# Optimization experiments

Hardware: AMD Instinct MI355X
Metric: run time of the kernel (lower is better)

The kernel has to match this reference:

```python
import jax, jax.numpy as jnp
import numpy as np

EMBED = 1024
HEADS = 16
HEAD_DIM = EMBED // HEADS


def setup_inputs() -> dict:
    key = jax.random.key(0)
    ks = jax.random.split(key, 8)
    N, S, E = 4, 2048, EMBED
    inp = {
        "queries": jax.random.normal(ks[0], (N, S, E), dtype=jnp.float32),
        "keys": jax.random.normal(ks[1], (N, S, E), dtype=jnp.float32),
        "values": jax.random.normal(ks[2], (N, S, E), dtype=jnp.float32),
        # projection weights, stored as (in, out) so y = x @ W
        "Wq": jax.random.normal(ks[3], (E, E), dtype=jnp.float32) / np.sqrt(E),
        "Wk": jax.random.normal(ks[4], (E, E), dtype=jnp.float32) / np.sqrt(E),
        "Wv": jax.random.normal(ks[5], (E, E), dtype=jnp.float32) / np.sqrt(E),
        "Wo": jax.random.normal(ks[6], (E, E), dtype=jnp.float32) / np.sqrt(E),
        "bo": jax.random.normal(ks[7], (E,), dtype=jnp.float32) * 0.01,
    }
    return inp


def reference(queries, keys, values, Wq, Wk, Wv, Wo, bo):
    N, Sq, E = queries.shape
    Sk = keys.shape[1]
    H, D = HEADS, HEAD_DIM
    # linear projections (no bias)
    q = (queries @ Wq).reshape(N, Sq, H, D)
    k = (keys @ Wk).reshape(N, Sk, H, D)
    v = (values @ Wv).reshape(N, Sk, H, D)
    # energy: [N, H, Sq, Sk]
    energy = jnp.einsum("nqhd,nkhd->nhqk", q, k)
    attn = jax.nn.softmax(energy / np.sqrt(D).astype(np.float32), axis=3)
    # out: [N, Sq, H, D] -> [N, Sq, E]
    out = jnp.einsum("nhqk,nkhd->nqhd", attn, v).reshape(N, Sq, E)
    return out @ Wo + bo
```

## Files before the change

kernel.cpp:

```cpp
#include <hip/hip_runtime.h>
#include <hip/hip_bf16.h>

typedef __bf16 bf16;
typedef bf16 bf16x4v __attribute__((ext_vector_type(4)));
typedef bf16 bf16x8 __attribute__((ext_vector_type(8)));
typedef float f32x4 __attribute__((ext_vector_type(4)));
typedef float f32x16 __attribute__((ext_vector_type(16)));
typedef unsigned int uint;
typedef unsigned short ushort;

static constexpr int E   = 1024;
static constexpr int SEQ = 2048;
static constexpr int NB  = 4;
static constexpr int M   = NB * SEQ;

__device__ __forceinline__ void async16(const void* g, void* l) {
  __builtin_amdgcn_global_load_lds(
      (const __attribute__((address_space(1))) void*)g,
      (__attribute__((address_space(3))) void*)l, 16, 0, 0);
}

__device__ __forceinline__ uint pack2(float a, float b) {
  bf16 x = (bf16)a, y = (bf16)b;
  return (uint)__builtin_bit_cast(ushort, x) |
         ((uint)__builtin_bit_cast(ushort, y) << 16);
}

__global__ __launch_bounds__(256) void k_prep(const float* q_in, const float* k_in,
                                              const float* v_in,
                                              bf16* qc, bf16* kc, bf16* vc,
                                              const float* W0, const float* W1,
                                              const float* W2, const float* W3,
                                              bf16* T0, bf16* T1, bf16* T2, bf16* T3) {
  __shared__ float tile[64][65];
  const int bid = blockIdx.x, t = threadIdx.x;
  if (bid < 12288) {
    const int z = bid >> 12, x = bid & 4095;
    const float* src = z == 0 ? q_in : z == 1 ? k_in : v_in;
    bf16* dst        = z == 0 ? qc   : z == 1 ? kc   : vc;
    size_t i = (size_t)x * 256 + t;
    const float4* s = reinterpret_cast<const float4*>(src) + i * 2;
    float4 a = s[0], b = s[1];
    bf16x8 o;
    o[0] = (bf16)a.x; o[1] = (bf16)a.y; o[2] = (bf16)a.z; o[3] = (bf16)a.w;
    o[4] = (bf16)b.x; o[5] = (bf16)b.y; o[6] = (bf16)b.z; o[7] = (bf16)b.w;
    *reinterpret_cast<bf16x8*>(dst + i * 8) = o;
  } else {
    const int wid = bid - 12288;
    const int wz = wid >> 8, rem = wid & 255;
    const int bx = rem & 15, by = rem >> 4;
    const float* W = wz == 0 ? W0 : wz == 1 ? W1 : wz == 2 ? W2 : W3;
    bf16* WT       = wz == 0 ? T0 : wz == 1 ? T1 : wz == 2 ? T2 : T3;
    const int tx = t & 63, ty = t >> 6;
    const int nb = bx * 64, kb = by * 64;
#pragma unroll
    for (int r = 0; r < 16; ++r)
      tile[ty + r * 4][tx] = W[(size_t)(kb + ty + r * 4) * E + nb + tx];
    __syncthreads();
#pragma unroll
    for (int r = 0; r < 16; ++r)
      WT[(size_t)(nb + ty + r * 4) * E + kb + tx] = (bf16)tile[tx][ty + r * 4];
  }
}

__global__ __launch_bounds__(256) void k_gemmP(const bf16* A0, const bf16* A1,
                                               const bf16* A2,
                                               const bf16* B0, const bf16* B1,
                                               const bf16* B2,
                                               bf16* O0, bf16* O1, bf16* O2) {
  __shared__ __align__(16) bf16 As[2][128 * 32];
  __shared__ __align__(16) bf16 Bs[2][128 * 32];
  const int z = blockIdx.z;
  const bf16* A  = z == 0 ? A0 : z == 1 ? A1 : A2;
  const bf16* BT = z == 0 ? B0 : z == 1 ? B1 : B2;
  const int t = threadIdx.x;
  const int l = t & 63, w = t >> 6;
  const int lo = l & 15, hi = l >> 4;
  const int wm = w >> 1, wn = w & 1;
  const int m0 = blockIdx.x * 128, n0 = blockIdx.y * 128;
  f32x4 acc[4][4] = {};

  const int r0 = t >> 2, s0 = t & 3;
  const bf16* ga0 = A + (size_t)(m0 + r0) * E + s0 * 8;
  const bf16* ga1 = ga0 + (size_t)64 * E;
  const bf16* gb0 = BT + (size_t)(n0 + r0) * E + s0 * 8;
  const bf16* gb1 = gb0 + (size_t)64 * E;

  auto stage = [&](int buf, int kk) {
    char* la = (char*)As[buf] + t * 16;
    char* lb = (char*)Bs[buf] + t * 16;
    async16(ga0 + kk, la);
    async16(ga1 + kk, la + 4096);
    async16(gb0 + kk, lb);
    async16(gb1 + kk, lb + 4096);
  };

  stage(0, 0);
  __syncthreads();
  int cur = 0;
  for (int kk = 0; kk < E; kk += 32) {
    if (kk + 32 < E) stage(cur ^ 1, kk + 32);
    const bf16* AsC = As[cur];
    const bf16* BsC = Bs[cur];
    bf16x8 af[4], bfr[4];
#pragma unroll
    for (int mi = 0; mi < 4; ++mi)
      af[mi] = *(const bf16x8*)&AsC[(wm * 64 + mi * 16 + lo) * 32 + hi * 8];
#pragma unroll
    for (int ni = 0; ni < 4; ++ni)
      bfr[ni] = *(const bf16x8*)&BsC[(wn * 64 + ni * 16 + lo) * 32 + hi * 8];
    __builtin_amdgcn_s_setprio(1);
#pragma unroll
    for (int mi = 0; mi < 4; ++mi)
#pragma unroll
      for (int ni = 0; ni < 4; ++ni)
        acc[mi][ni] = __builtin_amdgcn_mfma_f32_16x16x32_bf16(af[mi], bfr[ni],
                                                              acc[mi][ni], 0, 0, 0);
    __builtin_amdgcn_s_setprio(0);
    __syncthreads();
    cur ^= 1;
  }

  const int mrow = m0 + wm * 64, ncol = n0 + wn * 64;
  if (z == 2) {
#pragma unroll
    for (int mi = 0; mi < 4; ++mi) {
      int mrow_ = mrow + mi * 16 + hi * 4;
      int nb_ = mrow_ >> 11, sidx = mrow_ & 2047;
#pragma unroll
      for (int ni = 0; ni < 4; ++ni) {
        int col = ncol + ni * 16 + lo;
        bf16x4v v4;
#pragma unroll
        for (int j = 0; j < 4; ++j) v4[j] = (bf16)acc[mi][ni][j];
        *(bf16x4v*)(O2 + ((size_t)(nb_ * 16 + (col >> 6)) * 64 + (col & 63)) * SEQ + sidx) = v4;
      }
    }
  } else {
    const float sc = (z == 0) ? 0.18033688011112042f : 1.0f;
    bf16* C = z == 0 ? O0 : O1;
#pragma unroll
    for (int mi = 0; mi < 4; ++mi)
#pragma unroll
      for (int ni = 0; ni < 4; ++ni)
#pragma unroll
        for (int i = 0; i < 4; ++i)
          C[(size_t)(mrow + mi * 16 + hi * 4 + i) * E + ncol + ni * 16 + lo] =
              (bf16)(acc[mi][ni][i] * sc);
  }
}

__global__ __launch_bounds__(256) void k_gemmO(const bf16* __restrict__ A,
                                               const bf16* __restrict__ BT,
                                               float* __restrict__ C,
                                               const float* __restrict__ bias) {
  __shared__ __align__(16) bf16 As[2][128 * 32];
  __shared__ __align__(16) bf16 Bs[2][128 * 32];
  const int t = threadIdx.x;
  const int l = t & 63, w = t >> 6;
  const int lo = l & 15, hi = l >> 4;
  const int wm = w >> 1, wn = w & 1;
  const int m0 = blockIdx.x * 128, n0 = blockIdx.y * 128;
  f32x4 acc[4][4] = {};

  const int r0 = t >> 2, s0 = t & 3;
  const bf16* ga0 = A + (size_t)(m0 + r0) * E + s0 * 8;
  const bf16* ga1 = ga0 + (size_t)64 * E;
  const bf16* gb0 = BT + (size_t)(n0 + r0) * E + s0 * 8;
  const bf16* gb1 = gb0 + (size_t)64 * E;

  auto stage = [&](int buf, int kk) {
    char* la = (char*)As[buf] + t * 16;
    char* lb = (char*)Bs[buf] + t * 16;
    async16(ga0 + kk, la);
    async16(ga1 + kk, la + 4096);
    async16(gb0 + kk, lb);
    async16(gb1 + kk, lb + 4096);
  };

  stage(0, 0);
  __syncthreads();
  int cur = 0;
  for (int kk = 0; kk < E; kk += 32) {
    if (kk + 32 < E) stage(cur ^ 1, kk + 32);
    const bf16* AsC = As[cur];
    const bf16* BsC = Bs[cur];
    bf16x8 af[4], bfr[4];
#pragma unroll
    for (int mi = 0; mi < 4; ++mi)
      af[mi] = *(const bf16x8*)&AsC[(wm * 64 + mi * 16 + lo) * 32 + hi * 8];
#pragma unroll
    for (int ni = 0; ni < 4; ++ni)
      bfr[ni] = *(const bf16x8*)&BsC[(wn * 64 + ni * 16 + lo) * 32 + hi * 8];
    __builtin_amdgcn_s_setprio(1);
#pragma unroll
    for (int mi = 0; mi < 4; ++mi)
#pragma unroll
      for (int ni = 0; ni < 4; ++ni)
        acc[mi][ni] = __builtin_amdgcn_mfma_f32_16x16x32_bf16(af[mi], bfr[ni],
                                                              acc[mi][ni], 0, 0, 0);
    __builtin_amdgcn_s_setprio(0);
    __syncthreads();
    cur ^= 1;
  }

  const int mrow = m0 + wm * 64, ncol = n0 + wn * 64;
  float bv[4];
#pragma unroll
  for (int ni = 0; ni < 4; ++ni) bv[ni] = bias[ncol + ni * 16 + lo];
#pragma unroll
  for (int mi = 0; mi < 4; ++mi)
#pragma unroll
    for (int ni = 0; ni < 4; ++ni)
#pragma unroll
      for (int i = 0; i < 4; ++i)
        C[(size_t)(mrow + mi * 16 + hi * 4 + i) * E + ncol + ni * 16 + lo] =
            acc[mi][ni][i] + bv[ni];
}

__global__ __launch_bounds__(256, 2) void k_attn(const bf16* __restrict__ Qp,
                                                 const bf16* __restrict__ Kp,
                                                 const bf16* __restrict__ Vt,
                                                 bf16* __restrict__ Z) {
  __shared__ __align__(16) bf16 KV[2][2][64 * 64];
  const int t = threadIdx.x, l = t & 63, w = t >> 6;
  const int qq = l & 31, hi = l >> 5, l7 = l & 7;
  const int p = blockIdx.x;
  const int lswz = (p & 7) * 64 + (p >> 3);
  const int qb = lswz & 7, nh = lswz >> 3;
  const int n = nh >> 4, h = nh & 15;
  const int q0w = qb * 256 + w * 64;
  const int krow = (qq & 0x13) | ((qq & 4) << 1) | ((qq & 8) >> 1);

  bf16x8 qf[2][4];
#pragma unroll
  for (int j = 0; j < 2; ++j) {
    const bf16* qrow = Qp + (size_t)(n * SEQ + q0w + j * 32 + qq) * E + h * 64;
#pragma unroll
    for (int ks = 0; ks < 4; ++ks) qf[j][ks] = *(const bf16x8*)(qrow + ks * 16 + hi * 8);
  }

  const bf16* kbase = Kp + (size_t)n * SEQ * E + h * 64;
  const bf16* vbase = Vt + (size_t)nh * 64 * SEQ;
  const int r_st = t >> 3, s_st = t & 7;
  const int gs = (s_st ^ (r_st & 7)) * 8;

  auto stage = [&](int buf, int kt) {
    char* lk = (char*)KV[buf][0] + t * 16;
    char* lv = (char*)KV[buf][1] + t * 16;
    async16(kbase + (size_t)(kt + r_st) * E + gs, lk);
    async16(kbase + (size_t)(kt + r_st + 32) * E + gs, lk + 4096);
    async16(vbase + (size_t)r_st * SEQ + kt + gs, lv);
    async16(vbase + (size_t)(r_st + 32) * SEQ + kt + gs, lv + 4096);
  };

  f32x16 oacc[2][2] = {};
  float l_r[2] = {0.f, 0.f};

  stage(0, 0);
  __syncthreads();
  int cur = 0;
  for (int kt = 0; kt < SEQ; kt += 64) {
    if (kt + 64 < SEQ) stage(cur ^ 1, kt + 64);
    const bf16* KsC = KV[cur][0];
    const bf16* VsC = KV[cur][1];

    f32x16 sacc[2][2];
    __builtin_amdgcn_s_setprio(1);
#pragma unroll
    for (int kb = 0; kb < 2; ++kb) {
      bf16x8 kfr[4];
#pragma unroll
      for (int ks = 0; ks < 4; ++ks)
        kfr[ks] = *(const bf16x8*)(KsC + (kb * 32 + krow) * 64 + (((ks * 2 + hi) ^ (krow & 7)) * 8));
#pragma unroll
      for (int j = 0; j < 2; ++j) {
        f32x16 a = {};
#pragma unroll
        for (int ks = 0; ks < 4; ++ks)
          a = __builtin_amdgcn_mfma_f32_32x32x16_bf16(kfr[ks], qf[j][ks], a, 0, 0, 0);
        sacc[j][kb] = a;
      }
    }
    __builtin_amdgcn_s_setprio(0);

    uint wv[2][2][8];
#pragma unroll
    for (int j = 0; j < 2; ++j) {
      float rs = 0.f;
#pragma unroll
      for (int kb = 0; kb < 2; ++kb) {
        float pv[16];
#pragma unroll
        for (int r = 0; r < 16; ++r) {
          float e = __builtin_amdgcn_exp2f(sacc[j][kb][r]);
          pv[r] = e;
          rs += e;
        }
#pragma unroll
        for (int i = 0; i < 8; ++i) wv[j][kb][i] = pack2(pv[2 * i], pv[2 * i + 1]);
      }
      l_r[j] += rs;
    }

    __builtin_amdgcn_s_setprio(1);
#pragma unroll
    for (int d = 0; d < 2; ++d)
#pragma unroll
      for (int kb = 0; kb < 2; ++kb)
#pragma unroll
        for (int ks2 = 0; ks2 < 2; ++ks2) {
          const int ks = kb * 2 + ks2;
          bf16x8 vf = *(const bf16x8*)(VsC + (d * 32 + qq) * 64 + (((ks * 2 + hi) ^ l7) * 8));
#pragma unroll
          for (int j = 0; j < 2; ++j) {
            bf16x8 pf;
            uint* pp = (uint*)&pf;
            pp[0] = wv[j][kb][ks2 * 4 + 0];
            pp[1] = wv[j][kb][ks2 * 4 + 1];
            pp[2] = wv[j][kb][ks2 * 4 + 2];
            pp[3] = wv[j][kb][ks2 * 4 + 3];
            oacc[j][d] = __builtin_amdgcn_mfma_f32_32x32x16_bf16(vf, pf, oacc[j][d], 0, 0, 0);
          }
        }
    __builtin_amdgcn_s_setprio(0);
    __syncthreads();
    cur ^= 1;
  }

#pragma unroll
  for (int j = 0; j < 2; ++j) {
    const float lt = l_r[j] + __shfl_xor(l_r[j], 32);
    const float inv = 1.f / lt;
    bf16* zrow = Z + (size_t)(n * SEQ + q0w + j * 32 + qq) * E + h * 64;
#pragma unroll
    for (int d = 0; d < 2; ++d)
#pragma unroll
      for (int g = 0; g < 4; ++g) {
        bf16x4v v4;
#pragma unroll
        for (int jj = 0; jj < 4; ++jj) v4[jj] = (bf16)(oacc[j][d][g * 4 + jj] * inv);
        *(bf16x4v*)(zrow + d * 32 + g * 8 + hi * 4) = v4;
      }
  }
}

extern "C" void kernel_launch(void* const* d_in, const int* in_sizes, int n_in,
                              void* d_out, int out_size, void* d_ws, size_t ws_size,
                              hipStream_t stream) {
  const float* q_in = (const float*)d_in[0];
  const float* k_in = (const float*)d_in[1];
  const float* v_in = (const float*)d_in[2];
  const float* Wq   = (const float*)d_in[3];
  const float* Wk   = (const float*)d_in[4];
  const float* Wv   = (const float*)d_in[5];
  const float* Wo   = (const float*)d_in[6];
  const float* bo   = (const float*)d_in[7];

  char* ws = (char*)d_ws;
  const size_t SZ = (size_t)M * E * 2;
  bf16* qc   = (bf16*)(ws);
  bf16* kc   = (bf16*)(ws + SZ);
  bf16* vc   = (bf16*)(ws + 2 * SZ);
  bf16* qp   = (bf16*)(ws + 3 * SZ);
  bf16* kp   = (bf16*)(ws + 4 * SZ);
  bf16* vt   = (bf16*)(ws + 5 * SZ);
  bf16* zz   = (bf16*)(ws + 6 * SZ);
  bf16* wT   = (bf16*)(ws + 7 * SZ);
  bf16* wqT = wT;
  bf16* wkT = wT + (size_t)E * E;
  bf16* wvT = wT + 2 * (size_t)E * E;
  bf16* woT = wT + 3 * (size_t)E * E;

  dim3 b256(256);
  k_prep<<<dim3(13312), b256, 0, stream>>>(q_in, k_in, v_in, qc, kc, vc,
                                           Wq, Wk, Wv, Wo, wqT, wkT, wvT, woT);
  k_gemmP<<<dim3(64, 8, 3), b256, 0, stream>>>(qc, kc, vc, wqT, wkT, wvT,
                                               qp, kp, vt);
  k_attn<<<dim3(512), b256, 0, stream>>>(qp, kp, vt, zz);
  k_gemmO<<<dim3(64, 8), b256, 0, stream>>>(zz, woT, (float*)d_out, bo);
}
```

Measured before the change: 201.3 us.

## Split attention key sequence across two wave groups per block and merge via LDS

Doubles the attention block to 512 threads. Each group of four waves handles half of the key/value sequence with its own double-buffered LDS staging. At the end, the second half writes its partial outputs and row sums to LDS, and the first half adds them, normalizes and stores. This doubles the waves available per CU to hide latency on a grid that only fills two blocks per CU. The cost is more LDS per block, an extra merge step, and a tighter register budget from __launch_bounds__(512,4), which could cause spills.

Result: slower. 600.5 us (+198.4%).

```diff
diff --git a/kernel.cpp b/kernel.cpp
--- a/kernel.cpp
+++ b/kernel.cpp
@@ -218,18 +218,21 @@
             acc[mi][ni][i] + bv[ni];
 }
 
-__global__ __launch_bounds__(256, 2) void k_attn(const bf16* __restrict__ Qp,
+__global__ __launch_bounds__(512, 4) void k_attn(const bf16* __restrict__ Qp,
                                                  const bf16* __restrict__ Kp,
                                                  const bf16* __restrict__ Vt,
                                                  bf16* __restrict__ Z) {
-  __shared__ __align__(16) bf16 KV[2][2][64 * 64];
+  __shared__ __align__(16) char smem[65536];
   const int t = threadIdx.x, l = t & 63, w = t >> 6;
+  const int half = w >> 2, w4 = w & 3;
+  const int th = t & 255;
   const int qq = l & 31, hi = l >> 5, l7 = l & 7;
   const int p = blockIdx.x;
   const int lswz = (p & 7) * 64 + (p >> 3);
   const int qb = lswz & 7, nh = lswz >> 3;
   const int n = nh >> 4, h = nh & 15;
-  const int q0w = qb * 256 + w * 64;
+  const int q0w = qb * 256 + w4 * 64;
+  const int ktbase = half * (SEQ / 2);
   const int krow = (qq & 0x13) | ((qq & 4) << 1) | ((qq & 8) >> 1);
 
   bf16x8 qf[2][4];
@@ -242,16 +245,17 @@
 
   const bf16* kbase = Kp + (size_t)n * SEQ * E + h * 64;
   const bf16* vbase = Vt + (size_t)nh * 64 * SEQ;
-  const int r_st = t >> 3, s_st = t & 7;
+  const int r_st = th >> 3, s_st = th & 7;
   const int gs = (s_st ^ (r_st & 7)) * 8;
 
-  auto stage = [&](int buf, int kt) {
-    char* lk = (char*)KV[buf][0] + t * 16;
-    char* lv = (char*)KV[buf][1] + t * 16;
-    async16(kbase + (size_t)(kt + r_st) * E + gs, lk);
-    async16(kbase + (size_t)(kt + r_st + 32) * E + gs, lk + 4096);
-    async16(vbase + (size_t)r_st * SEQ + kt + gs, lv);
-    async16(vbase + (size_t)(r_st + 32) * SEQ + kt + gs, lv + 4096);
+  auto stage = [&](int buf, int ktl) {
+    char* lk = smem + half * 32768 + buf * 16384 + th * 16;
+    char* lv = lk + 8192;
+    const int ktg = ktbase + ktl;
+    async16(kbase + (size_t)(ktg + r_st) * E + gs, lk);
+    async16(kbase + (size_t)(ktg + r_st + 32) * E + gs, lk + 4096);
+    async16(vbase + (size_t)r_st * SEQ + ktg + gs, lv);
+    async16(vbase + (size_t)(r_st + 32) * SEQ + ktg + gs, lv + 4096);
   };
 
   f32x16 oacc[2][2] = {};
@@ -260,10 +264,10 @@
   stage(0, 0);
   __syncthreads();
   int cur = 0;
-  for (int kt = 0; kt < SEQ; kt += 64) {
-    if (kt + 64 < SEQ) stage(cur ^ 1, kt + 64);
-    const bf16* KsC = KV[cur][0];
-    const bf16* VsC = KV[cur][1];
+  for (int ktl = 0; ktl < SEQ / 2; ktl += 64) {
+    if (ktl + 64 < SEQ / 2) stage(cur ^ 1, ktl + 64);
+    const bf16* KsC = (const bf16*)(smem + half * 32768 + cur * 16384);
+    const bf16* VsC = (const bf16*)(smem + half * 32768 + cur * 16384 + 8192);
 
     f32x16 sacc[2][2];
     __builtin_amdgcn_s_setprio(1);
@@ -328,20 +332,39 @@
     cur ^= 1;
   }
 
+  float lt[2];
+#pragma unroll
+  for (int j = 0; j < 2; ++j) lt[j] = l_r[j] + __shfl_xor(l_r[j], 32);
+
+  float* Obuf = (float*)smem;
 #pragma unroll
   for (int j = 0; j < 2; ++j) {
-    const float lt = l_r[j] + __shfl_xor(l_r[j], 32);
-    const float inv = 1.f / lt;
-    bf16* zrow = Z + (size_t)(n * SEQ + q0w + j * 32 + qq) * E + h * 64;
-#pragma unroll
-    for (int d = 0; d < 2; ++d)
-#pragma unroll
-      for (int g = 0; g < 4; ++g) {
-        bf16x4v v4;
-#pragma unroll
-        for (int jj = 0; jj < 4; ++jj) v4[jj] = (bf16)(oacc[j][d][g * 4 + jj] * inv);
-        *(bf16x4v*)(zrow + d * 32 + g * 8 + hi * 4) = v4;
-      }
+    float* row = Obuf + (w4 * 64 + l) * 36;
+    if (half == 1) {
+      *(f32x16*)(row) = oacc[j][0];
+      *(f32x16*)(row + 16) = oacc[j][1];
+      row[32] = lt[j];
+    }
+    __syncthreads();
+    if (half == 0) {
+      f32x16 o1a = *(const f32x16*)(row);
+      f32x16 o1b = *(const f32x16*)(row + 16);
+      const float inv = 1.f / (lt[j] + row[32]);
+      f32x16 fo[2];
+      fo[0] = (oacc[j][0] + o1a) * inv;
+      fo[1] = (oacc[j][1] + o1b) * inv;
+      bf16* zrow = Z + (size_t)(n * SEQ + q0w + j * 32 + qq) * E + h * 64;
+#pragma unroll
+      for (int d = 0; d < 2; ++d)
+#pragma unroll
+        for (int g = 0; g < 4; ++g) {
+          bf16x4v v4;
+#pragma unroll
+          for (int jj = 0; jj < 4; ++jj) v4[jj] = (bf16)fo[d][g * 4 + jj];
+          *(bf16x4v*)(zrow + d * 32 + g * 8 + hi * 4) = v4;
+        }
+    }
+    if (j == 0) __syncthreads();
   }
 }
 
@@ -377,6 +400,6 @@
                                            Wq, Wk, Wv, Wo, wqT, wkT, wvT, woT);
   k_gemmP<<<dim3(64, 8, 3), b256, 0, stream>>>(qc, kc, vc, wqT, wkT, wvT,
                                                qp, kp, vt);
-  k_attn<<<dim3(512), b256, 0, stream>>>(qp, kp, vt, zz);
+  k_attn<<<dim3(512), dim3(512), 0, stream>>>(qp, kp, vt, zz);
   k_gemmO<<<dim3(64, 8), b256, 0, stream>>>(zz, woT, (float*)d_out, bo);
 }
```

## Fuse fp32-to-bf16 input conversion into projection GEMM A-operand loads

Applied to the files above, without the earlier changes.

Removes the separate pass that converts the fp32 query/key/value inputs to bf16. The projection GEMM now reads fp32 activations straight from global memory into registers and packs them to bf16 for the MFMA A operand, dropping A from shared memory. This saves a full write and re-read of three 8M-element bf16 buffers. In exchange, each block's A reads are uncached, per-wave fp32 register loads that are not shared through LDS, and these loads are not prefetched ahead of the compute.

After: 305.3 us. +51.7%, slower.

```diff
diff --git a/kernel.cpp b/kernel.cpp
--- a/kernel.cpp
+++ b/kernel.cpp
@@ -26,52 +26,34 @@
          ((uint)__builtin_bit_cast(ushort, y) << 16);
 }
 
-__global__ __launch_bounds__(256) void k_prep(const float* q_in, const float* k_in,
-                                              const float* v_in,
-                                              bf16* qc, bf16* kc, bf16* vc,
-                                              const float* W0, const float* W1,
+__global__ __launch_bounds__(256) void k_prep(const float* W0, const float* W1,
                                               const float* W2, const float* W3,
                                               bf16* T0, bf16* T1, bf16* T2, bf16* T3) {
   __shared__ float tile[64][65];
   const int bid = blockIdx.x, t = threadIdx.x;
-  if (bid < 12288) {
-    const int z = bid >> 12, x = bid & 4095;
-    const float* src = z == 0 ? q_in : z == 1 ? k_in : v_in;
-    bf16* dst        = z == 0 ? qc   : z == 1 ? kc   : vc;
-    size_t i = (size_t)x * 256 + t;
-    const float4* s = reinterpret_cast<const float4*>(src) + i * 2;
-    float4 a = s[0], b = s[1];
-    bf16x8 o;
-    o[0] = (bf16)a.x; o[1] = (bf16)a.y; o[2] = (bf16)a.z; o[3] = (bf16)a.w;
-    o[4] = (bf16)b.x; o[5] = (bf16)b.y; o[6] = (bf16)b.z; o[7] = (bf16)b.w;
-    *reinterpret_cast<bf16x8*>(dst + i * 8) = o;
-  } else {
-    const int wid = bid - 12288;
-    const int wz = wid >> 8, rem = wid & 255;
-    const int bx = rem & 15, by = rem >> 4;
-    const float* W = wz == 0 ? W0 : wz == 1 ? W1 : wz == 2 ? W2 : W3;
-    bf16* WT       = wz == 0 ? T0 : wz == 1 ? T1 : wz == 2 ? T2 : T3;
-    const int tx = t & 63, ty = t >> 6;
-    const int nb = bx * 64, kb = by * 64;
-#pragma unroll
-    for (int r = 0; r < 16; ++r)
-      tile[ty + r * 4][tx] = W[(size_t)(kb + ty + r * 4) * E + nb + tx];
-    __syncthreads();
-#pragma unroll
-    for (int r = 0; r < 16; ++r)
-      WT[(size_t)(nb + ty + r * 4) * E + kb + tx] = (bf16)tile[tx][ty + r * 4];
-  }
-}
-
-__global__ __launch_bounds__(256) void k_gemmP(const bf16* A0, const bf16* A1,
-                                               const bf16* A2,
+  const int wz = bid >> 8, rem = bid & 255;
+  const int bx = rem & 15, by = rem >> 4;
+  const float* W = wz == 0 ? W0 : wz == 1 ? W1 : wz == 2 ? W2 : W3;
+  bf16* WT       = wz == 0 ? T0 : wz == 1 ? T1 : wz == 2 ? T2 : T3;
+  const int tx = t & 63, ty = t >> 6;
+  const int nb = bx * 64, kb = by * 64;
+#pragma unroll
+  for (int r = 0; r < 16; ++r)
+    tile[ty + r * 4][tx] = W[(size_t)(kb + ty + r * 4) * E + nb + tx];
+  __syncthreads();
+#pragma unroll
+  for (int r = 0; r < 16; ++r)
+    WT[(size_t)(nb + ty + r * 4) * E + kb + tx] = (bf16)tile[tx][ty + r * 4];
+}
+
+__global__ __launch_bounds__(256) void k_gemmP(const float* A0, const float* A1,
+                                               const float* A2,
                                                const bf16* B0, const bf16* B1,
                                                const bf16* B2,
                                                bf16* O0, bf16* O1, bf16* O2) {
-  __shared__ __align__(16) bf16 As[2][128 * 32];
   __shared__ __align__(16) bf16 Bs[2][128 * 32];
   const int z = blockIdx.z;
-  const bf16* A  = z == 0 ? A0 : z == 1 ? A1 : A2;
+  const float* A = z == 0 ? A0 : z == 1 ? A1 : A2;
   const bf16* BT = z == 0 ? B0 : z == 1 ? B1 : B2;
   const int t = threadIdx.x;
   const int l = t & 63, w = t >> 6;
@@ -81,31 +63,36 @@
   f32x4 acc[4][4] = {};
 
   const int r0 = t >> 2, s0 = t & 3;
-  const bf16* ga0 = A + (size_t)(m0 + r0) * E + s0 * 8;
-  const bf16* ga1 = ga0 + (size_t)64 * E;
   const bf16* gb0 = BT + (size_t)(n0 + r0) * E + s0 * 8;
   const bf16* gb1 = gb0 + (size_t)64 * E;
 
-  auto stage = [&](int buf, int kk) {
-    char* la = (char*)As[buf] + t * 16;
+  auto stageB = [&](int buf, int kk) {
     char* lb = (char*)Bs[buf] + t * 16;
-    async16(ga0 + kk, la);
-    async16(ga1 + kk, la + 4096);
     async16(gb0 + kk, lb);
     async16(gb1 + kk, lb + 4096);
   };
 
-  stage(0, 0);
+  const float* ga[4];
+#pragma unroll
+  for (int mi = 0; mi < 4; ++mi)
+    ga[mi] = A + (size_t)(m0 + wm * 64 + mi * 16 + lo) * E + hi * 8;
+
+  stageB(0, 0);
   __syncthreads();
   int cur = 0;
   for (int kk = 0; kk < E; kk += 32) {
-    if (kk + 32 < E) stage(cur ^ 1, kk + 32);
-    const bf16* AsC = As[cur];
+    if (kk + 32 < E) stageB(cur ^ 1, kk + 32);
+    bf16x8 af[4], bfr[4];
+#pragma unroll
+    for (int mi = 0; mi < 4; ++mi) {
+      float4 a0 = *(const float4*)(ga[mi] + kk);
+      float4 a1 = *(const float4*)(ga[mi] + kk + 4);
+      uint4 wq;
+      wq.x = pack2(a0.x, a0.y); wq.y = pack2(a0.z, a0.w);
+      wq.z = pack2(a1.x, a1.y); wq.w = pack2(a1.z, a1.w);
+      af[mi] = __builtin_bit_cast(bf16x8, wq);
+    }
     const bf16* BsC = Bs[cur];
-    bf16x8 af[4], bfr[4];
-#pragma unroll
-    for (int mi = 0; mi < 4; ++mi)
-      af[mi] = *(const bf16x8*)&AsC[(wm * 64 + mi * 16 + lo) * 32 + hi * 8];
 #pragma unroll
     for (int ni = 0; ni < 4; ++ni)
       bfr[ni] = *(const bf16x8*)&BsC[(wn * 64 + ni * 16 + lo) * 32 + hi * 8];
@@ -359,23 +346,19 @@
 
   char* ws = (char*)d_ws;
   const size_t SZ = (size_t)M * E * 2;
-  bf16* qc   = (bf16*)(ws);
-  bf16* kc   = (bf16*)(ws + SZ);
-  bf16* vc   = (bf16*)(ws + 2 * SZ);
-  bf16* qp   = (bf16*)(ws + 3 * SZ);
-  bf16* kp   = (bf16*)(ws + 4 * SZ);
-  bf16* vt   = (bf16*)(ws + 5 * SZ);
-  bf16* zz   = (bf16*)(ws + 6 * SZ);
-  bf16* wT   = (bf16*)(ws + 7 * SZ);
+  bf16* qp = (bf16*)(ws);
+  bf16* kp = (bf16*)(ws + SZ);
+  bf16* vt = (bf16*)(ws + 2 * SZ);
+  bf16* zz = (bf16*)(ws + 3 * SZ);
+  bf16* wT = (bf16*)(ws + 4 * SZ);
   bf16* wqT = wT;
   bf16* wkT = wT + (size_t)E * E;
   bf16* wvT = wT + 2 * (size_t)E * E;
   bf16* woT = wT + 3 * (size_t)E * E;
 
   dim3 b256(256);
-  k_prep<<<dim3(13312), b256, 0, stream>>>(q_in, k_in, v_in, qc, kc, vc,
-                                           Wq, Wk, Wv, Wo, wqT, wkT, wvT, woT);
-  k_gemmP<<<dim3(64, 8, 3), b256, 0, stream>>>(qc, kc, vc, wqT, wkT, wvT,
+  k_prep<<<dim3(1024), b256, 0, stream>>>(Wq, Wk, Wv, Wo, wqT, wkT, wvT, woT);
+  k_gemmP<<<dim3(64, 8, 3), b256, 0, stream>>>(q_in, k_in, v_in, wqT, wkT, wvT,
                                                qp, kp, vt);
   k_attn<<<dim3(512), b256, 0, stream>>>(qp, kp, vt, zz);
   k_gemmO<<<dim3(64, 8), b256, 0, stream>>>(zz, woT, (float*)d_out, bo);
```

## Software-pipeline attention QK/PV across triple-buffered tiles and XCD-swizzle GEMM grids

Applied to the files above, without the earlier changes.

The attention kernel moves to three LDS buffers and a skewed loop. Each iteration computes QK^T for the current tile, then PV for the previous tile, then softmax, so exp work can overlap with MFMA work. The row-sum accumulation is split into four partial sums to shorten the dependency chain. Both GEMM kernels switch to a 1D grid that is remapped so that consecutive blocks on the same XCD share M rows, which should improve L2 reuse. The extra buffer raises LDS use to 48KB per block, which may limit occupancy at 2 blocks/CU, and the extra live registers for the probabilities raise register pressure.

After: 200.9 us. About the same (-0.2%).

```diff
diff --git a/kernel.cpp b/kernel.cpp
--- a/kernel.cpp
+++ b/kernel.cpp
@@ -70,14 +70,17 @@
                                                bf16* O0, bf16* O1, bf16* O2) {
   __shared__ __align__(16) bf16 As[2][128 * 32];
   __shared__ __align__(16) bf16 Bs[2][128 * 32];
-  const int z = blockIdx.z;
+  const int id = blockIdx.x;
+  const int xcd = id & 7, rq = id >> 3;
+  const int z = rq >> 6, rr = rq & 63;
+  const int m0 = (xcd * 8 + (rr >> 3)) * 128;
+  const int n0 = (rr & 7) * 128;
   const bf16* A  = z == 0 ? A0 : z == 1 ? A1 : A2;
   const bf16* BT = z == 0 ? B0 : z == 1 ? B1 : B2;
   const int t = threadIdx.x;
   const int l = t & 63, w = t >> 6;
   const int lo = l & 15, hi = l >> 4;
   const int wm = w >> 1, wn = w & 1;
-  const int m0 = blockIdx.x * 128, n0 = blockIdx.y * 128;
   f32x4 acc[4][4] = {};
 
   const int r0 = t >> 2, s0 = t & 3;
@@ -156,11 +159,14 @@
                                                const float* __restrict__ bias) {
   __shared__ __align__(16) bf16 As[2][128 * 32];
   __shared__ __align__(16) bf16 Bs[2][128 * 32];
+  const int id = blockIdx.x;
+  const int xcd = id & 7, rq = id >> 3;
+  const int m0 = (xcd * 8 + (rq >> 3)) * 128;
+  const int n0 = (rq & 7) * 128;
   const int t = threadIdx.x;
   const int l = t & 63, w = t >> 6;
   const int lo = l & 15, hi = l >> 4;
   const int wm = w >> 1, wn = w & 1;
-  const int m0 = blockIdx.x * 128, n0 = blockIdx.y * 128;
   f32x4 acc[4][4] = {};
 
   const int r0 = t >> 2, s0 = t & 3;
@@ -222,7 +228,8 @@
                                                  const bf16* __restrict__ Kp,
                                                  const bf16* __restrict__ Vt,
                                                  bf16* __restrict__ Z) {
-  __shared__ __align__(16) bf16 KV[2][2][64 * 64];
+  __shared__ __align__(16) bf16 KV[3][2][64 * 64];
+  char* smbase = (char*)KV;
   const int t = threadIdx.x, l = t & 63, w = t >> 6;
   const int qq = l & 31, hi = l >> 5, l7 = l & 7;
   const int p = blockIdx.x;
@@ -245,9 +252,9 @@
   const int r_st = t >> 3, s_st = t & 7;
   const int gs = (s_st ^ (r_st & 7)) * 8;
 
-  auto stage = [&](int buf, int kt) {
-    char* lk = (char*)KV[buf][0] + t * 16;
-    char* lv = (char*)KV[buf][1] + t * 16;
+  auto stage = [&](int off, int kt) {
+    char* lk = smbase + off + t * 16;
+    char* lv = smbase + off + 8192 + t * 16;
     async16(kbase + (size_t)(kt + r_st) * E + gs, lk);
     async16(kbase + (size_t)(kt + r_st + 32) * E + gs, lk + 4096);
     async16(vbase + (size_t)r_st * SEQ + kt + gs, lv);
@@ -256,16 +263,11 @@
 
   f32x16 oacc[2][2] = {};
   float l_r[2] = {0.f, 0.f};
-
-  stage(0, 0);
-  __syncthreads();
-  int cur = 0;
-  for (int kt = 0; kt < SEQ; kt += 64) {
-    if (kt + 64 < SEQ) stage(cur ^ 1, kt + 64);
-    const bf16* KsC = KV[cur][0];
-    const bf16* VsC = KV[cur][1];
-
-    f32x16 sacc[2][2];
+  f32x16 sacc[2][2];
+  uint pw[2][2][8];
+
+  auto qkt = [&](int off) {
+    const bf16* KsC = (const bf16*)(smbase + off);
     __builtin_amdgcn_s_setprio(1);
 #pragma unroll
     for (int kb = 0; kb < 2; ++kb) {
@@ -283,26 +285,30 @@
       }
     }
     __builtin_amdgcn_s_setprio(0);
-
-    uint wv[2][2][8];
+  };
+
+  auto smx = [&]() {
 #pragma unroll
     for (int j = 0; j < 2; ++j) {
-      float rs = 0.f;
+      float rs[4] = {0.f, 0.f, 0.f, 0.f};
 #pragma unroll
       for (int kb = 0; kb < 2; ++kb) {
-        float pv[16];
+        float pvv[16];
 #pragma unroll
         for (int r = 0; r < 16; ++r) {
           float e = __builtin_amdgcn_exp2f(sacc[j][kb][r]);
-          pv[r] = e;
-          rs += e;
+          pvv[r] = e;
+          rs[r & 3] += e;
         }
 #pragma unroll
-        for (int i = 0; i < 8; ++i) wv[j][kb][i] = pack2(pv[2 * i], pv[2 * i + 1]);
+        for (int i = 0; i < 8; ++i) pw[j][kb][i] = pack2(pvv[2 * i], pvv[2 * i + 1]);
       }
-      l_r[j] += rs;
+      l_r[j] += (rs[0] + rs[1]) + (rs[2] + rs[3]);
     }
-
+  };
+
+  auto pvx = [&](int off) {
+    const bf16* VsC = (const bf16*)(smbase + off + 8192);
     __builtin_amdgcn_s_setprio(1);
 #pragma unroll
     for (int d = 0; d < 2; ++d)
@@ -316,17 +322,34 @@
           for (int j = 0; j < 2; ++j) {
             bf16x8 pf;
             uint* pp = (uint*)&pf;
-            pp[0] = wv[j][kb][ks2 * 4 + 0];
-            pp[1] = wv[j][kb][ks2 * 4 + 1];
-            pp[2] = wv[j][kb][ks2 * 4 + 2];
-            pp[3] = wv[j][kb][ks2 * 4 + 3];
+            pp[0] = pw[j][kb][ks2 * 4 + 0];
+            pp[1] = pw[j][kb][ks2 * 4 + 1];
+            pp[2] = pw[j][kb][ks2 * 4 + 2];
+            pp[3] = pw[j][kb][ks2 * 4 + 3];
             oacc[j][d] = __builtin_amdgcn_mfma_f32_32x32x16_bf16(vf, pf, oacc[j][d], 0, 0, 0);
           }
         }
     __builtin_amdgcn_s_setprio(0);
+  };
+
+  stage(0, 0);
+  __syncthreads();
+  stage(16384, 64);
+  qkt(0);
+  smx();
+  __syncthreads();
+
+  int pOff = 0, cOff = 16384, nOff = 32768;
+  for (int kt = 64; kt < SEQ; kt += 64) {
+    if (kt + 64 < SEQ) stage(nOff, kt + 64);
+    qkt(cOff);
+    pvx(pOff);
+    smx();
     __syncthreads();
-    cur ^= 1;
-  }
+    const int tmp = pOff;
+    pOff = cOff; cOff = nOff; nOff = tmp;
+  }
+  pvx(pOff);
 
 #pragma unroll
   for (int j = 0; j < 2; ++j) {
@@ -375,8 +398,8 @@
   dim3 b256(256);
   k_prep<<<dim3(13312), b256, 0, stream>>>(q_in, k_in, v_in, qc, kc, vc,
                                            Wq, Wk, Wv, Wo, wqT, wkT, wvT, woT);
-  k_gemmP<<<dim3(64, 8, 3), b256, 0, stream>>>(qc, kc, vc, wqT, wkT, wvT,
-                                               qp, kp, vt);
+  k_gemmP<<<dim3(1536), b256, 0, stream>>>(qc, kc, vc, wqT, wkT, wvT,
+                                           qp, kp, vt);
   k_attn<<<dim3(512), b256, 0, stream>>>(qp, kp, vt, zz);
-  k_gemmO<<<dim3(64, 8), b256, 0, stream>>>(zz, woT, (float*)d_out, bo);
-}
+  k_gemmO<<<dim3(512), b256, 0, stream>>>(zz, woT, (float*)d_out, bo);
+}
```
